# Optimization experiments

Measured on AMD Instinct MI355X. Metric: run time of the kernel, lower is better.

Reference implementation:

```python
import jax, jax.numpy as jnp
import numpy as np

N_NODES = 100000
N_EDGES = 1_600_000
D = 32


def setup_inputs() -> dict:
    key = jax.random.key(0)
    k1, k2, k3, k4, k5 = jax.random.split(key, 5)
    x = jax.random.normal(k1, (N_NODES, D), dtype=jnp.float32)
    W1 = jax.random.normal(k2, (D, D), dtype=jnp.float32) * (1.0 / np.sqrt(D))
    W2 = jax.random.normal(k3, (D, D), dtype=jnp.float32) * (1.0 / np.sqrt(D))
    b2 = jax.random.normal(k4, (D,), dtype=jnp.float32) * 0.01
    edge_index = jax.random.randint(k5, (2, N_EDGES), 0, N_NODES, dtype=jnp.int64)
    return {"x": x, "W1": W1, "W2": W2, "b2": b2, "edge_index": edge_index}


def reference(x, W1, W2, b2, edge_index):
    # ptensors0.transfer0 over the graph: F1[i] = sum_{(j->i) in E} x[j]
    src = edge_index[0]
    dst = edge_index[1]
    F1 = jax.ops.segment_sum(x[src], dst, num_segments=x.shape[0])  # [N, D]
    # out = lin2(x) + lin1(F1)  (lin2 has bias, lin1 does not; torch Linear: y = x @ W.T + b)
    return x @ W2.T + b2 + F1 @ W1.T
```

## Files before the change

### kernel.cpp

```cpp
#include <hip/hip_runtime.h>
#include <hip/hip_bf16.h>

#define DIM 32
#define LOG_NPB 7
#define NPB 128
#define CAP 4096
#define NBINS 800
#define EPB 4096
#define EPT 16

__global__ __launch_bounds__(256) void fused_lin_kernel(
    const float* __restrict__ x,
    const float* __restrict__ W1,
    const float* __restrict__ W2,
    const float* __restrict__ b2,
    float* __restrict__ out,
    unsigned* __restrict__ y32,
    int* __restrict__ cursor, int nb,
    int n_nodes)
{
    __shared__ float W1s[DIM][DIM];
    __shared__ float W2s[DIM][DIM];
    __shared__ float b2s[DIM];
    __shared__ float xs[8][DIM];

    const int t = threadIdx.x;

    if (blockIdx.x == 0) {
        for (int i = t; i < nb; i += 256) cursor[i] = i * CAP;
    }

    for (int i = t; i < DIM * DIM; i += 256) {
        int c = i >> 5, k = i & 31;
        W1s[k][c] = W1[i];
        W2s[k][c] = W2[i];
    }
    if (t < DIM) b2s[t] = b2[t];

    const int r = t >> 5;
    const int c = t & 31;
    const int ntiles = (n_nodes + 7) >> 3;

    for (int tile = blockIdx.x; tile < ntiles; tile += gridDim.x) {
        const int row = tile * 8 + r;
        __syncthreads();
        if (row < n_nodes) xs[r][c] = x[(long)row * DIM + c];
        __syncthreads();
        if (row < n_nodes) {
            float a2 = b2s[c];
            float a1 = 0.0f;
            #pragma unroll
            for (int k = 0; k < DIM; ++k) {
                float xv = xs[r][k];
                a2 += xv * W2s[k][c];
                a1 += xv * W1s[k][c];
            }
            out[(long)row * DIM + c] = a2;
            float hi = __shfl_down(a1, 1);
            if ((c & 1) == 0) {
                __hip_bfloat16 blo = __float2bfloat16(a1);
                __hip_bfloat16 bhi = __float2bfloat16(hi);
                unsigned pack = ((unsigned)(*(unsigned short*)&bhi) << 16)
                              | (unsigned)(*(unsigned short*)&blo);
                y32[(size_t)row * 16 + (c >> 1)] = pack;
            }
        }
    }
}

__global__ __launch_bounds__(256) void bucket_scatter_kernel(
    const int* __restrict__ src, const int* __restrict__ dst,
    int* __restrict__ cursor, unsigned* __restrict__ bedges, int nE)
{
    __shared__ int cnt[NBINS];
    __shared__ int base[NBINS];
    __shared__ int rank[NBINS];

    const int t = threadIdx.x;
    const long blockStart = (long)blockIdx.x * EPB;

    for (int i = t; i < NBINS; i += 256) { cnt[i] = 0; rank[i] = 0; }
    __syncthreads();

    int es[EPT], ed[EPT];
    #pragma unroll
    for (int i = 0; i < EPT; ++i) {
        long e = blockStart + i * 256 + t;
        if (e < nE) { es[i] = src[e]; ed[i] = dst[e]; }
        else        { es[i] = -1;     ed[i] = 0;      }
    }
    #pragma unroll
    for (int i = 0; i < EPT; ++i) {
        if (es[i] >= 0) atomicAdd(&cnt[ed[i] >> LOG_NPB], 1);
    }
    __syncthreads();

    for (int i = t; i < NBINS; i += 256) {
        int c = cnt[i];
        if (c > 0) base[i] = atomicAdd(&cursor[i], c);
    }
    __syncthreads();

    #pragma unroll
    for (int i = 0; i < EPT; ++i) {
        if (es[i] >= 0) {
            int b = ed[i] >> LOG_NPB;
            int r = atomicAdd(&rank[b], 1);
            int p = base[b] + r;
            if (p < (b + 1) * CAP)
                bedges[p] = ((unsigned)es[i] << LOG_NPB) | (unsigned)(ed[i] & (NPB - 1));
        }
    }
}

__global__ __launch_bounds__(512) void sort_gather_kernel(
    const int* __restrict__ cursor, const unsigned* __restrict__ bedges,
    const unsigned short* __restrict__ yb,
    float* __restrict__ out, int n_nodes)
{
    __shared__ unsigned ent[CAP];
    __shared__ unsigned sorted[CAP];
    __shared__ int cnt[NPB];
    __shared__ int ex[NPB];
    __shared__ int cur[NPB];

    const int b = blockIdx.x;
    const int t = threadIdx.x;
    const int start = b * CAP;
    int n = cursor[b] - start;
    if (n > CAP) n = CAP;
    if (n < 0) n = 0;

    if (t < NPB) { cnt[t] = 0; cur[t] = 0; }
    __syncthreads();

    for (int i = t; i < n; i += 512) {
        unsigned e = bedges[start + i];
        ent[i] = e;
        atomicAdd(&cnt[e & (NPB - 1)], 1);
    }
    __syncthreads();

    if (t < NPB) ex[t] = cnt[t];
    __syncthreads();
    for (int off = 1; off < NPB; off <<= 1) {
        int add = 0;
        if (t < NPB && t >= off) add = ex[t - off];
        __syncthreads();
        if (t < NPB) ex[t] += add;
        __syncthreads();
    }
    if (t < NPB) ex[t] -= cnt[t];
    __syncthreads();

    for (int i = t; i < n; i += 512) {
        unsigned e = ent[i];
        int bin = (int)(e & (NPB - 1));
        int r = atomicAdd(&cur[bin], 1);
        sorted[ex[bin] + r] = e >> LOG_NPB;
    }
    __syncthreads();

    const int wv   = t >> 6;
    const int lane = t & 63;
    const int slot = lane >> 3;
    const int li   = lane & 7;

    int ln   = wv;
    int node = b * NPB + ln;
    if (node >= n_nodes) return;

    int st = ex[ln];
    int d  = cnt[ln];
    int s[4];
    #pragma unroll
    for (int k = 0; k < 4; ++k) {
        int e = slot + 8 * k;
        int idx = (e < d) ? e : (d > 0 ? d - 1 : 0);
        s[k] = (int)sorted[(d > 0 ? st : 0) + idx];
    }
    float4 o = make_float4(0.f, 0.f, 0.f, 0.f);
    if (slot == 0) o = ((const float4*)(out + ((size_t)node << 5)))[li];

    while (true) {
        const bool big = d > 16;
        ushort4 u[4];
        u[0] = *(const ushort4*)(yb + ((size_t)s[0] << 5) + (li << 2));
        u[1] = *(const ushort4*)(yb + ((size_t)s[1] << 5) + (li << 2));
        if (big) {
            u[2] = *(const ushort4*)(yb + ((size_t)s[2] << 5) + (li << 2));
            u[3] = *(const ushort4*)(yb + ((size_t)s[3] << 5) + (li << 2));
        }

        const int ln_n   = ln + 8;
        const int node_n = node + 8;
        const bool have_n = (ln_n < NPB) && (node_n < n_nodes);
        int st_n = 0, d_n = 0;
        int sn[4];
        float4 o_n = make_float4(0.f, 0.f, 0.f, 0.f);
        if (have_n) {
            st_n = ex[ln_n];
            d_n  = cnt[ln_n];
            #pragma unroll
            for (int k = 0; k < 4; ++k) {
                int e = slot + 8 * k;
                int idx = (e < d_n) ? e : (d_n > 0 ? d_n - 1 : 0);
                sn[k] = (int)sorted[(d_n > 0 ? st_n : 0) + idx];
            }
            if (slot == 0) o_n = ((const float4*)(out + ((size_t)node_n << 5)))[li];
        }

        float a0 = 0.f, a1 = 0.f, a2 = 0.f, a3 = 0.f;
        #pragma unroll
        for (int k = 0; k < 2; ++k) {
            const bool v = (slot + 8 * k) < d;
            a0 += v ? __uint_as_float((unsigned)u[k].x << 16) : 0.f;
            a1 += v ? __uint_as_float((unsigned)u[k].y << 16) : 0.f;
            a2 += v ? __uint_as_float((unsigned)u[k].z << 16) : 0.f;
            a3 += v ? __uint_as_float((unsigned)u[k].w << 16) : 0.f;
        }
        if (big) {
            #pragma unroll
            for (int k = 2; k < 4; ++k) {
                const bool v = (slot + 8 * k) < d;
                a0 += v ? __uint_as_float((unsigned)u[k].x << 16) : 0.f;
                a1 += v ? __uint_as_float((unsigned)u[k].y << 16) : 0.f;
                a2 += v ? __uint_as_float((unsigned)u[k].z << 16) : 0.f;
                a3 += v ? __uint_as_float((unsigned)u[k].w << 16) : 0.f;
            }
            for (int e0 = 32 + slot; e0 < d; e0 += 8) {
                int ss = (int)sorted[st + e0];
                ushort4 uu = *(const ushort4*)(yb + ((size_t)ss << 5) + (li << 2));
                a0 += __uint_as_float((unsigned)uu.x << 16);
                a1 += __uint_as_float((unsigned)uu.y << 16);
                a2 += __uint_as_float((unsigned)uu.z << 16);
                a3 += __uint_as_float((unsigned)uu.w << 16);
            }
        }

        #pragma unroll
        for (int m = 8; m < 64; m <<= 1) {
            a0 += __shfl_xor(a0, m);
            a1 += __shfl_xor(a1, m);
            a2 += __shfl_xor(a2, m);
            a3 += __shfl_xor(a3, m);
        }

        if (slot == 0 && d > 0) {
            float4 w;
            w.x = o.x + a0; w.y = o.y + a1; w.z = o.z + a2; w.w = o.w + a3;
            ((float4*)(out + ((size_t)node << 5)))[li] = w;
        }

        if (!have_n) break;
        ln = ln_n; node = node_n; st = st_n; d = d_n;
        s[0] = sn[0]; s[1] = sn[1]; s[2] = sn[2]; s[3] = sn[3];
        o = o_n;
    }
}

extern "C" void kernel_launch(void* const* d_in, const int* in_sizes, int n_in,
                              void* d_out, int out_size, void* d_ws, size_t ws_size,
                              hipStream_t stream) {
    const float* x  = (const float*)d_in[0];
    const float* W1 = (const float*)d_in[1];
    const float* W2 = (const float*)d_in[2];
    const float* b2 = (const float*)d_in[3];
    const int*   ei = (const int*)d_in[4];

    const int n_nodes = in_sizes[0] / DIM;
    const int n_edges = in_sizes[4] / 2;
    const int* src = ei;
    const int* dst = ei + n_edges;
    float* out = (float*)d_out;

    const int nb = (n_nodes + NPB - 1) / NPB;

    char* basep = (char*)d_ws;
    size_t off = 0;
    auto alloc = [&](size_t bytes) {
        char* p = basep + off;
        off = (off + bytes + 255) & ~(size_t)255;
        return p;
    };
    unsigned* y32    = (unsigned*)alloc((size_t)n_nodes * DIM * sizeof(unsigned short));
    int*      cursor = (int*)     alloc((size_t)nb * sizeof(int));
    unsigned* bedges = (unsigned*)alloc((size_t)nb * CAP * sizeof(unsigned));
    (void)ws_size;

    fused_lin_kernel<<<1024, 256, 0, stream>>>(x, W1, W2, b2, out, y32, cursor, nb, n_nodes);
    bucket_scatter_kernel<<<(n_edges + EPB - 1) / EPB, 256, 0, stream>>>(src, dst, cursor, bedges, n_edges);
    sort_gather_kernel<<<nb, 512, 0, stream>>>(cursor, bedges, (const unsigned short*)y32, out, n_nodes);
}
```

Before: 82.78 us.

## Merge linear and edge-bucketing kernels into one launch with role-split blocks

Folds the dense linear pass and the edge bucket-scatter pass into a single kernel where the first blocks bucket edges and the rest compute the two linear projections, so both independent phases run concurrently and one launch boundary disappears. Cursor initialisation moves to a memset and cursors become per-bucket relative offsets. The gather loop is also generalised so row loads are predicated per chunk instead of a two-level big/small branch. Costs are the extra memset call and higher shared memory per block from the union of both phases' arrays, which may reduce occupancy.

```diff
diff --git a/kernel.cpp b/kernel.cpp
--- a/kernel.cpp
+++ b/kernel.cpp
@@ -8,17 +8,22 @@
 #define NBINS 800
 #define EPB 4096
 #define EPT 16
-
-__global__ __launch_bounds__(256) void fused_lin_kernel(
+#define LIN_BLOCKS 1024
+
+__global__ __launch_bounds__(256) void lin_scatter_kernel(
     const float* __restrict__ x,
     const float* __restrict__ W1,
     const float* __restrict__ W2,
     const float* __restrict__ b2,
     float* __restrict__ out,
     unsigned* __restrict__ y32,
-    int* __restrict__ cursor, int nb,
-    int n_nodes)
+    const int* __restrict__ src, const int* __restrict__ dst,
+    int* __restrict__ cursor, unsigned* __restrict__ bedges,
+    int nE, int n_nodes, int nScat)
 {
+    __shared__ int cnt[NBINS];
+    __shared__ int base[NBINS];
+    __shared__ int rank[NBINS];
     __shared__ float W1s[DIM][DIM];
     __shared__ float W2s[DIM][DIM];
     __shared__ float b2s[DIM];
@@ -26,89 +31,80 @@
 
     const int t = threadIdx.x;
 
-    if (blockIdx.x == 0) {
-        for (int i = t; i < nb; i += 256) cursor[i] = i * CAP;
-    }
-
-    for (int i = t; i < DIM * DIM; i += 256) {
-        int c = i >> 5, k = i & 31;
-        W1s[k][c] = W1[i];
-        W2s[k][c] = W2[i];
-    }
-    if (t < DIM) b2s[t] = b2[t];
-
-    const int r = t >> 5;
-    const int c = t & 31;
-    const int ntiles = (n_nodes + 7) >> 3;
-
-    for (int tile = blockIdx.x; tile < ntiles; tile += gridDim.x) {
-        const int row = tile * 8 + r;
-        __syncthreads();
-        if (row < n_nodes) xs[r][c] = x[(long)row * DIM + c];
-        __syncthreads();
-        if (row < n_nodes) {
-            float a2 = b2s[c];
-            float a1 = 0.0f;
-            #pragma unroll
-            for (int k = 0; k < DIM; ++k) {
-                float xv = xs[r][k];
-                a2 += xv * W2s[k][c];
-                a1 += xv * W1s[k][c];
-            }
-            out[(long)row * DIM + c] = a2;
-            float hi = __shfl_down(a1, 1);
-            if ((c & 1) == 0) {
-                __hip_bfloat16 blo = __float2bfloat16(a1);
-                __hip_bfloat16 bhi = __float2bfloat16(hi);
-                unsigned pack = ((unsigned)(*(unsigned short*)&bhi) << 16)
-                              | (unsigned)(*(unsigned short*)&blo);
-                y32[(size_t)row * 16 + (c >> 1)] = pack;
-            }
-        }
-    }
-}
-
-__global__ __launch_bounds__(256) void bucket_scatter_kernel(
-    const int* __restrict__ src, const int* __restrict__ dst,
-    int* __restrict__ cursor, unsigned* __restrict__ bedges, int nE)
-{
-    __shared__ int cnt[NBINS];
-    __shared__ int base[NBINS];
-    __shared__ int rank[NBINS];
-
-    const int t = threadIdx.x;
-    const long blockStart = (long)blockIdx.x * EPB;
-
-    for (int i = t; i < NBINS; i += 256) { cnt[i] = 0; rank[i] = 0; }
-    __syncthreads();
-
-    int es[EPT], ed[EPT];
-    #pragma unroll
-    for (int i = 0; i < EPT; ++i) {
-        long e = blockStart + i * 256 + t;
-        if (e < nE) { es[i] = src[e]; ed[i] = dst[e]; }
-        else        { es[i] = -1;     ed[i] = 0;      }
-    }
-    #pragma unroll
-    for (int i = 0; i < EPT; ++i) {
-        if (es[i] >= 0) atomicAdd(&cnt[ed[i] >> LOG_NPB], 1);
-    }
-    __syncthreads();
-
-    for (int i = t; i < NBINS; i += 256) {
-        int c = cnt[i];
-        if (c > 0) base[i] = atomicAdd(&cursor[i], c);
-    }
-    __syncthreads();
-
-    #pragma unroll
-    for (int i = 0; i < EPT; ++i) {
-        if (es[i] >= 0) {
-            int b = ed[i] >> LOG_NPB;
-            int r = atomicAdd(&rank[b], 1);
-            int p = base[b] + r;
-            if (p < (b + 1) * CAP)
-                bedges[p] = ((unsigned)es[i] << LOG_NPB) | (unsigned)(ed[i] & (NPB - 1));
+    if (blockIdx.x < nScat) {
+        const long blockStart = (long)blockIdx.x * EPB;
+
+        for (int i = t; i < NBINS; i += 256) { cnt[i] = 0; rank[i] = 0; }
+        __syncthreads();
+
+        int es[EPT], ed[EPT];
+        #pragma unroll
+        for (int i = 0; i < EPT; ++i) {
+            long e = blockStart + i * 256 + t;
+            if (e < nE) { es[i] = src[e]; ed[i] = dst[e]; }
+            else        { es[i] = -1;     ed[i] = 0;      }
+        }
+        #pragma unroll
+        for (int i = 0; i < EPT; ++i) {
+            if (es[i] >= 0) atomicAdd(&cnt[ed[i] >> LOG_NPB], 1);
+        }
+        __syncthreads();
+
+        for (int i = t; i < NBINS; i += 256) {
+            int c = cnt[i];
+            if (c > 0) base[i] = atomicAdd(&cursor[i], c);
+        }
+        __syncthreads();
+
+        #pragma unroll
+        for (int i = 0; i < EPT; ++i) {
+            if (es[i] >= 0) {
+                int b = ed[i] >> LOG_NPB;
+                int r = atomicAdd(&rank[b], 1);
+                int p = base[b] + r;
+                if (p < CAP)
+                    bedges[b * CAP + p] =
+                        ((unsigned)es[i] << LOG_NPB) | (unsigned)(ed[i] & (NPB - 1));
+            }
+        }
+    } else {
+        const int lb = blockIdx.x - nScat;
+
+        for (int i = t; i < DIM * DIM; i += 256) {
+            int c = i >> 5, k = i & 31;
+            W1s[k][c] = W1[i];
+            W2s[k][c] = W2[i];
+        }
+        if (t < DIM) b2s[t] = b2[t];
+
+        const int r = t >> 5;
+        const int c = t & 31;
+        const int ntiles = (n_nodes + 7) >> 3;
+
+        for (int tile = lb; tile < ntiles; tile += LIN_BLOCKS) {
+            const int row = tile * 8 + r;
+            __syncthreads();
+            if (row < n_nodes) xs[r][c] = x[(long)row * DIM + c];
+            __syncthreads();
+            if (row < n_nodes) {
+                float a2 = b2s[c];
+                float a1 = 0.0f;
+                #pragma unroll
+                for (int k = 0; k < DIM; ++k) {
+                    float xv = xs[r][k];
+                    a2 += xv * W2s[k][c];
+                    a1 += xv * W1s[k][c];
+                }
+                out[(long)row * DIM + c] = a2;
+                float hi = __shfl_down(a1, 1);
+                if ((c & 1) == 0) {
+                    __hip_bfloat16 blo = __float2bfloat16(a1);
+                    __hip_bfloat16 bhi = __float2bfloat16(hi);
+                    unsigned pack = ((unsigned)(*(unsigned short*)&bhi) << 16)
+                                  | (unsigned)(*(unsigned short*)&blo);
+                    y32[(size_t)row * 16 + (c >> 1)] = pack;
+                }
+            }
         }
     }
 }
@@ -127,7 +123,7 @@
     const int b = blockIdx.x;
     const int t = threadIdx.x;
     const int start = b * CAP;
-    int n = cursor[b] - start;
+    int n = cursor[b];
     if (n > CAP) n = CAP;
     if (n < 0) n = 0;
 
@@ -183,13 +179,11 @@
     if (slot == 0) o = ((const float4*)(out + ((size_t)node << 5)))[li];
 
     while (true) {
-        const bool big = d > 16;
         ushort4 u[4];
-        u[0] = *(const ushort4*)(yb + ((size_t)s[0] << 5) + (li << 2));
-        u[1] = *(const ushort4*)(yb + ((size_t)s[1] << 5) + (li << 2));
-        if (big) {
-            u[2] = *(const ushort4*)(yb + ((size_t)s[2] << 5) + (li << 2));
-            u[3] = *(const ushort4*)(yb + ((size_t)s[3] << 5) + (li << 2));
+        #pragma unroll
+        for (int k = 0; k < 4; ++k) {
+            if (8 * k < d)
+                u[k] = *(const ushort4*)(yb + ((size_t)s[k] << 5) + (li << 2));
         }
 
         const int ln_n   = ln + 8;
@@ -212,30 +206,22 @@
 
         float a0 = 0.f, a1 = 0.f, a2 = 0.f, a3 = 0.f;
         #pragma unroll
-        for (int k = 0; k < 2; ++k) {
-            const bool v = (slot + 8 * k) < d;
-            a0 += v ? __uint_as_float((unsigned)u[k].x << 16) : 0.f;
-            a1 += v ? __uint_as_float((unsigned)u[k].y << 16) : 0.f;
-            a2 += v ? __uint_as_float((unsigned)u[k].z << 16) : 0.f;
-            a3 += v ? __uint_as_float((unsigned)u[k].w << 16) : 0.f;
-        }
-        if (big) {
-            #pragma unroll
-            for (int k = 2; k < 4; ++k) {
+        for (int k = 0; k < 4; ++k) {
+            if (8 * k < d) {
                 const bool v = (slot + 8 * k) < d;
                 a0 += v ? __uint_as_float((unsigned)u[k].x << 16) : 0.f;
                 a1 += v ? __uint_as_float((unsigned)u[k].y << 16) : 0.f;
                 a2 += v ? __uint_as_float((unsigned)u[k].z << 16) : 0.f;
                 a3 += v ? __uint_as_float((unsigned)u[k].w << 16) : 0.f;
             }
-            for (int e0 = 32 + slot; e0 < d; e0 += 8) {
-                int ss = (int)sorted[st + e0];
-                ushort4 uu = *(const ushort4*)(yb + ((size_t)ss << 5) + (li << 2));
-                a0 += __uint_as_float((unsigned)uu.x << 16);
-                a1 += __uint_as_float((unsigned)uu.y << 16);
-                a2 += __uint_as_float((unsigned)uu.z << 16);
-                a3 += __uint_as_float((unsigned)uu.w << 16);
-            }
+        }
+        for (int e0 = 32 + slot; e0 < d; e0 += 8) {
+            int ss = (int)sorted[st + e0];
+            ushort4 uu = *(const ushort4*)(yb + ((size_t)ss << 5) + (li << 2));
+            a0 += __uint_as_float((unsigned)uu.x << 16);
+            a1 += __uint_as_float((unsigned)uu.y << 16);
+            a2 += __uint_as_float((unsigned)uu.z << 16);
+            a3 += __uint_as_float((unsigned)uu.w << 16);
         }
 
         #pragma unroll
@@ -288,7 +274,12 @@
     unsigned* bedges = (unsigned*)alloc((size_t)nb * CAP * sizeof(unsigned));
     (void)ws_size;
 
-    fused_lin_kernel<<<1024, 256, 0, stream>>>(x, W1, W2, b2, out, y32, cursor, nb, n_nodes);
-    bucket_scatter_kernel<<<(n_edges + EPB - 1) / EPB, 256, 0, stream>>>(src, dst, cursor, bedges, n_edges);
-    sort_gather_kernel<<<nb, 512, 0, stream>>>(cursor, bedges, (const unsigned short*)y32, out, n_nodes);
+    hipMemsetAsync(cursor, 0, (size_t)nb * sizeof(int), stream);
+
+    const int nScat = (n_edges + EPB - 1) / EPB;
+    lin_scatter_kernel<<<nScat + LIN_BLOCKS, 256, 0, stream>>>(
+        x, W1, W2, b2, out, y32, src, dst, cursor, bedges, n_edges, n_nodes, nScat);
+
+    sort_gather_kernel<<<nb, 512, 0, stream>>>(cursor, bedges,
+                                               (const unsigned short*)y32, out, n_nodes);
 }
```

Result: no change. 83.86 us (+1.3%).
